# Kernel optimization log

Hardware: AMD Instinct MI355X
Metric: run time of the kernel (lower is better)

The kernel has to match this reference:

```python
import jax, jax.numpy as jnp
import numpy as np

NEG = -1000000.0

def setup_inputs() -> dict:
    key = jax.random.key(0)
    ks = jax.random.split(key, 7)
    B, Lq, Lk, Dq, Dk, Dv, H = 4, 256, 1024, 512, 512, 512, 256
    return {
        "query": jax.random.normal(ks[0], (B, Lq, Dq), dtype=jnp.float32),
        "key": jax.random.normal(ks[1], (B, Lk, Dk), dtype=jnp.float32),
        "value": jax.random.normal(ks[2], (B, Lk, Dv), dtype=jnp.float32),
        "valid_len": jax.random.randint(ks[3], (B,), 1, Lk + 1),
        "Wq": jax.random.normal(ks[4], (Dq, H), dtype=jnp.float32) * (1.0 / np.sqrt(Dq)),
        "Wk": jax.random.normal(ks[5], (Dk, H), dtype=jnp.float32) * (1.0 / np.sqrt(Dk)),
        "wv": jax.random.normal(ks[6], (H,), dtype=jnp.float32) * (1.0 / np.sqrt(H)),
    }

def reference(query, key, value, valid_len, Wq, Wk, wv):
    # projections: [B,Lq,H], [B,Lk,H]
    q = jnp.einsum("bqd,dh->bqh", query, Wq)
    k = jnp.einsum("bkd,dh->bkh", key, Wk)
    # broadcast-add + tanh: [B,Lq,Lk,H]
    features = jnp.tanh(q[:, :, None, :] + k[:, None, :, :])
    # score projection to scalar: [B,Lq,Lk]
    score = jnp.einsum("bqkh,h->bqk", features, wv)
    # masked softmax over keys (valid_len per batch, broadcast over queries)
    Lk = key.shape[1]
    mask = jnp.arange(Lk)[None, None, :] < valid_len[:, None, None]
    score = jnp.where(mask, score, NEG)
    attn = jax.nn.softmax(score, axis=-1)
    # weighted sum of values: [B,Lq,Dv]  (dropout is identity in eval)
    return jnp.einsum("bqk,bkv->bqv", attn, value)
```

## Files before the change

### kernel.cpp

```cpp
#include <hip/hip_runtime.h>

typedef __attribute__((ext_vector_type(8))) short short8v;
typedef __attribute__((ext_vector_type(4))) float float4v;
typedef unsigned int uint;

#define TWO_LOG2E 2.8853900817779268f
#define LOG2E     1.4426950408889634f

__device__ inline uint rne_bf16(float x) {
    uint u = __float_as_uint(x);
    return (u + 0x7fffu + ((u >> 16) & 1u)) >> 16;
}
__device__ inline uint pack_hi_lo(float a0, float a1, uint& lo_pack) {
    const uint h0 = rne_bf16(a0), h1 = rne_bf16(a1);
    const float f0 = __uint_as_float(h0 << 16), f1 = __uint_as_float(h1 << 16);
    const float l0 = a0 - f0, l1 = a1 - f1;
    lo_pack = (rne_bf16(l1) << 16) | rne_bf16(l0);
    return (h1 << 16) | h0;
}
__device__ inline void split8(const float4 x0, const float4 x1,
                              short8v& h, short8v& l) {
    const float xs[8] = {x0.x, x0.y, x0.z, x0.w, x1.x, x1.y, x1.z, x1.w};
    #pragma unroll
    for (int j = 0; j < 8; ++j) {
        const uint u = __float_as_uint(xs[j]);
        const uint hi = u & 0xFFFF0000u;
        const float lo = xs[j] - __uint_as_float(hi);
        h[j] = (short)(hi >> 16);
        l[j] = (short)rne_bf16(lo);
    }
}

__global__ __launch_bounds__(256) void prep_w(
    const float* __restrict__ Wq, const float* __restrict__ Wk,
    ushort* __restrict__ WT_hi, ushort* __restrict__ WT_lo)
{
    const int t = blockIdx.x * 256 + threadIdx.x;
    const int n = t & 255;
    const int kg = ((t >> 8) & 63) * 8;
    const int w = t >> 14;
    const float* W = w ? Wk : Wq;
    float x[8];
    #pragma unroll
    for (int i = 0; i < 8; ++i) x[i] = W[(size_t)(kg + i) * 256 + n];
    uint h0, h1, h2, h3, l0, l1, l2, l3;
    h0 = pack_hi_lo(x[0], x[1], l0);
    h1 = pack_hi_lo(x[2], x[3], l1);
    h2 = pack_hi_lo(x[4], x[5], l2);
    h3 = pack_hi_lo(x[6], x[7], l3);
    const size_t off = ((size_t)w * 256 + n) * 512 + kg;
    *(uint4*)(WT_hi + off) = make_uint4(h0, h1, h2, h3);
    *(uint4*)(WT_lo + off) = make_uint4(l0, l1, l2, l3);
}

__global__ __launch_bounds__(256) void prep_v(
    const float* __restrict__ value, const int* __restrict__ vlen,
    ushort* __restrict__ VT_hi, ushort* __restrict__ VT_lo)
{
    __shared__ float t[64][69];
    const int b = blockIdx.z;
    const int k0 = blockIdx.y * 64, n0 = blockIdx.x * 64;
    const int kendB = (vlen[b] + 31) & ~31;
    if (k0 >= kendB) return;

    const int tid = threadIdx.x;
    const int n_in = (tid & 15) * 4, k_in = tid >> 4;
    const float* src = value + ((size_t)b * 1024 + k0 + k_in) * 512 + n0 + n_in;
    #pragma unroll
    for (int p = 0; p < 4; ++p) {
        const float4 x = *(const float4*)(src + (size_t)p * 16 * 512);
        t[k_in + p * 16][n_in + 0] = x.x;
        t[k_in + p * 16][n_in + 1] = x.y;
        t[k_in + p * 16][n_in + 2] = x.z;
        t[k_in + p * 16][n_in + 3] = x.w;
    }
    __syncthreads();

    const int rn = tid >> 2, c0 = (tid & 3) * 16;
    uint hp[8], lp[8];
    #pragma unroll
    for (int i = 0; i < 8; ++i)
        hp[i] = pack_hi_lo(t[c0 + 2 * i][rn], t[c0 + 2 * i + 1][rn], lp[i]);
    const size_t off = ((size_t)b * 512 + n0 + rn) * 1024 + k0 + c0;
    *(uint4*)(VT_hi + off) = make_uint4(hp[0], hp[1], hp[2], hp[3]);
    *(uint4*)(VT_hi + off + 8) = make_uint4(hp[4], hp[5], hp[6], hp[7]);
    *(uint4*)(VT_lo + off) = make_uint4(lp[0], lp[1], lp[2], lp[3]);
    *(uint4*)(VT_lo + off + 8) = make_uint4(lp[4], lp[5], lp[6], lp[7]);
}

#define LOADA(s, kbase) { const int ko = (kbase) + half * 8;                   \
    _Pragma("unroll") for (int f = 0; f < 2; ++f) {                            \
        const float4 x0 = *(const float4*)(a_f + (size_t)(f * 16) * 512 + ko); \
        const float4 x1 = *(const float4*)(a_f + (size_t)(f * 16) * 512 + ko + 4); \
        split8(x0, x1, ah##s[f], al##s[f]); } }

#define LOADB(s, kbase) { const int ko = (kbase) + half * 8;                   \
    _Pragma("unroll") for (int f = 0; f < 4; ++f) {                            \
        bh##s[f] = *(const short8v*)(wt_h + (size_t)(f * 16) * 512 + ko);      \
        bl##s[f] = *(const short8v*)(wt_l + (size_t)(f * 16) * 512 + ko); } }

#define MFMAS(s)                                                                          \
    _Pragma("unroll") for (int mf = 0; mf < 2; ++mf)                                      \
    _Pragma("unroll") for (int nf = 0; nf < 4; ++nf) {                                    \
        acc[mf][nf] = __builtin_amdgcn_mfma_f32_16x16x32_bf16(ah##s[mf], bh##s[nf], acc[mf][nf], 0, 0, 0); \
        acc[mf][nf] = __builtin_amdgcn_mfma_f32_16x16x32_bf16(ah##s[mf], bl##s[nf], acc[mf][nf], 0, 0, 0); \
        acc[mf][nf] = __builtin_amdgcn_mfma_f32_16x16x32_bf16(al##s[mf], bh##s[nf], acc[mf][nf], 0, 0, 0); }

__global__ __launch_bounds__(64) void proj_mfma(
    const float* __restrict__ query, const float* __restrict__ key,
    const ushort* __restrict__ WT_hi, const ushort* __restrict__ WT_lo,
    const int* __restrict__ valid_len,
    float* __restrict__ EqT, float* __restrict__ EkT)
{
    const int lane = threadIdx.x;
    const int n0 = blockIdx.x * 64;
    const int m0 = blockIdx.y * 32;
    const bool isq = (m0 < 1024);
    int b = 0, kk0 = 0;
    if (!isq) {
        kk0 = (m0 - 1024) & 1023;
        b = (m0 - 1024) >> 10;
        if (kk0 >= valid_len[b]) return;
    }
    const int r = lane & 15, half = lane >> 4;
    const size_t wsel = isq ? 0 : (size_t)256 * 512;
    const ushort* wt_h = WT_hi + wsel + (size_t)(n0 + r) * 512;
    const ushort* wt_l = WT_lo + wsel + (size_t)(n0 + r) * 512;
    const float* a_f = isq ? (query + (size_t)(m0 + r) * 512)
                           : (key + (size_t)(m0 - 1024 + r) * 512);

    float4v acc[2][4] = {{{0.f}}};
    short8v ah0[2], al0[2], bh0[4], bl0[4];
    short8v ah1[2], al1[2], bh1[4], bl1[4];

    LOADA(0, 0); LOADB(0, 0);
    for (int kt = 0; kt < 512; kt += 64) {
        LOADA(1, kt + 32); LOADB(1, kt + 32);
        MFMAS(0);
        if (kt + 64 < 512) { LOADA(0, kt + 64); LOADB(0, kt + 64); }
        MFMAS(1);
    }

    #pragma unroll
    for (int mf = 0; mf < 2; ++mf) {
        #pragma unroll
        for (int nf = 0; nf < 4; ++nf) {
            float4v e;
            #pragma unroll
            for (int i = 0; i < 4; ++i)
                e[i] = __builtin_amdgcn_exp2f(acc[mf][nf][i] * TWO_LOG2E);
            if (isq) {
                *(float4v*)(EqT + (size_t)(n0 + nf * 16 + r) * 1024 +
                            m0 + mf * 16 + half * 4) = e;
            } else {
                *(float4v*)(EkT + (size_t)(b * 256 + n0 + nf * 16 + r) * 1024 +
                            kk0 + mf * 16 + half * 4) = e;
            }
        }
    }
}

__global__ __launch_bounds__(256) void score_partial(
    const float* __restrict__ EqT, const float* __restrict__ EkT,
    const float* __restrict__ wv, const int* __restrict__ valid_len,
    float* __restrict__ P)
{
    __shared__ float eqs[64][16];
    __shared__ float wvs[64];

    const int orig = blockIdx.x;
    const int wgid = (orig & 7) * 128 + (orig >> 3);
    const int qt = wgid & 15;
    const int kt = (wgid >> 4) & 3;
    const int hq = (wgid >> 6) & 3;
    const int b  = wgid >> 8;

    const int vlen = valid_len[b];
    if (kt * 256 >= vlen) return;

    const int tid = threadIdx.x;
    const int kg = tid & 63, qg = tid >> 6;
    const int k0 = kt * 256 + kg * 4;
    const int q0 = qt * 16;
    const int h0 = hq * 64;

    if (tid < 64) wvs[tid] = wv[h0 + tid];
    {
        const int i = tid * 4;
        const int h = i >> 4, q = i & 15;
        *(float4*)&eqs[h][q] =
            *(const float4*)(EqT + (size_t)(h0 + h) * 1024 + b * 256 + q0 + q);
    }
    __syncthreads();

    float acc[4][4] = {};
    if (k0 < vlen) {
        const float* ekp = EkT + (size_t)(b * 256 + h0) * 1024 + k0;
        #pragma unroll 2
        for (int h = 0; h < 64; ++h) {
            const float4 ek = *(const float4*)(ekp + (size_t)h * 1024);
            const float4 eq = *(const float4*)&eqs[h][qg * 4];
            const float w = wvs[h];
            const float ekv[4] = {ek.x, ek.y, ek.z, ek.w};
            const float eqv[4] = {eq.x, eq.y, eq.z, eq.w};
            #pragma unroll
            for (int qi = 0; qi < 4; ++qi) {
                const float e = eqv[qi];
                acc[qi][0] = fmaf(w, __builtin_amdgcn_rcpf(fmaf(e, ekv[0], 1.f)), acc[qi][0]);
                acc[qi][1] = fmaf(w, __builtin_amdgcn_rcpf(fmaf(e, ekv[1], 1.f)), acc[qi][1]);
                acc[qi][2] = fmaf(w, __builtin_amdgcn_rcpf(fmaf(e, ekv[2], 1.f)), acc[qi][2]);
                acc[qi][3] = fmaf(w, __builtin_amdgcn_rcpf(fmaf(e, ekv[3], 1.f)), acc[qi][3]);
            }
        }
    }

    float* Pq = P + (size_t)hq * (1024 * 1024);
    #pragma unroll
    for (int qi = 0; qi < 4; ++qi) {
        float4 o;
        o.x = acc[qi][0]; o.y = acc[qi][1]; o.z = acc[qi][2]; o.w = acc[qi][3];
        *(float4*)(Pq + (size_t)(b * 256 + q0 + qg * 4 + qi) * 1024 + k0) = o;
    }
}

__global__ __launch_bounds__(1024) void softmax_kernel(
    const float* __restrict__ P, const int* __restrict__ valid_len,
    ushort* __restrict__ attn_hi, ushort* __restrict__ attn_lo)
{
    __shared__ float red[16][4];

    const int tid = threadIdx.x;
    const int b = blockIdx.x >> 6;
    const int q0 = (blockIdx.x & 63) << 2;

    const int vlen = valid_len[b];
    const int k = tid;
    const bool v = (k < vlen);

    float s[4], m[4];
    #pragma unroll
    for (int q = 0; q < 4; ++q) {
        const size_t off = (size_t)(b * 256 + q0 + q) * 1024 + k;
        s[q] = -2.f * (P[off] + P[off + 1048576] +
                       P[off + 2097152] + P[off + 3145728]);
        m[q] = v ? s[q] : -1e30f;
    }
    #pragma unroll
    for (int o = 32; o; o >>= 1) {
        #pragma unroll
        for (int q = 0; q < 4; ++q) m[q] = fmaxf(m[q], __shfl_xor(m[q], o));
    }
    const int wid = tid >> 6;
    if ((tid & 63) == 0) {
        #pragma unroll
        for (int q = 0; q < 4; ++q) red[wid][q] = m[q];
    }
    __syncthreads();
    #pragma unroll
    for (int q = 0; q < 4; ++q) {
        float mm = red[0][q];
        #pragma unroll
        for (int w = 1; w < 16; ++w) mm = fmaxf(mm, red[w][q]);
        m[q] = mm;
    }
    __syncthreads();

    float p[4], l[4];
    #pragma unroll
    for (int q = 0; q < 4; ++q) {
        p[q] = v ? __builtin_amdgcn_exp2f((s[q] - m[q]) * LOG2E) : 0.f;
        l[q] = p[q];
    }
    #pragma unroll
    for (int o = 32; o; o >>= 1) {
        #pragma unroll
        for (int q = 0; q < 4; ++q) l[q] += __shfl_xor(l[q], o);
    }
    if ((tid & 63) == 0) {
        #pragma unroll
        for (int q = 0; q < 4; ++q) red[wid][q] = l[q];
    }
    __syncthreads();
    #pragma unroll
    for (int q = 0; q < 4; ++q) {
        float ss = red[0][q];
        #pragma unroll
        for (int w = 1; w < 16; ++w) ss += red[w][q];
        const float a = p[q] * __builtin_amdgcn_rcpf(ss);
        const uint hi = rne_bf16(a);
        const float lo = a - __uint_as_float(hi << 16);
        const size_t off = (size_t)(b * 256 + q0 + q) * 1024 + k;
        attn_hi[off] = (ushort)hi;
        attn_lo[off] = (ushort)rne_bf16(lo);
    }
}

#define PVLOAD(s, ko) {                                   \
    ah##s = *(const short8v*)(ah_p + (ko));               \
    al##s = *(const short8v*)(al_p + (ko));               \
    bh0##s = *(const short8v*)(bh_p + (ko));              \
    bl0##s = *(const short8v*)(bl_p + (ko));              \
    bh1##s = *(const short8v*)(bh_p + 16 * 1024 + (ko));  \
    bl1##s = *(const short8v*)(bl_p + 16 * 1024 + (ko)); }

#define PVMFMA(s) {                                                              \
    acc0 = __builtin_amdgcn_mfma_f32_16x16x32_bf16(ah##s, bh0##s, acc0, 0, 0, 0); \
    acc0 = __builtin_amdgcn_mfma_f32_16x16x32_bf16(ah##s, bl0##s, acc0, 0, 0, 0); \
    acc0 = __builtin_amdgcn_mfma_f32_16x16x32_bf16(al##s, bh0##s, acc0, 0, 0, 0); \
    acc1 = __builtin_amdgcn_mfma_f32_16x16x32_bf16(ah##s, bh1##s, acc1, 0, 0, 0); \
    acc1 = __builtin_amdgcn_mfma_f32_16x16x32_bf16(ah##s, bl1##s, acc1, 0, 0, 0); \
    acc1 = __builtin_amdgcn_mfma_f32_16x16x32_bf16(al##s, bh1##s, acc1, 0, 0, 0); }

__global__ __launch_bounds__(256) void pv_mfma(
    const ushort* __restrict__ attn_hi, const ushort* __restrict__ attn_lo,
    const ushort* __restrict__ VT_hi, const ushort* __restrict__ VT_lo,
    const int* __restrict__ valid_len,
    float* __restrict__ out)
{
    const int orig = blockIdx.x;
    const int wgid = (orig & 7) * 32 + (orig >> 3);
    const int qb = wgid & 3;
    const int rest = wgid >> 2;
    const int b = rest & 3;
    const int nt = rest >> 2;

    const int wid = threadIdx.x >> 6, lane = threadIdx.x & 63;
    const int n0 = nt * 32;
    const int q0 = qb * 64 + wid * 16;
    const int r = lane & 15, half = lane >> 4;
    const int kend = (valid_len[b] + 31) & ~31;

    const ushort* ah_p = attn_hi + (size_t)(b * 256 + q0 + r) * 1024 + half * 8;
    const ushort* al_p = attn_lo + (size_t)(b * 256 + q0 + r) * 1024 + half * 8;
    const ushort* bh_p = VT_hi + (size_t)(b * 512 + n0 + r) * 1024 + half * 8;
    const ushort* bl_p = VT_lo + (size_t)(b * 512 + n0 + r) * 1024 + half * 8;

    float4v acc0 = {0.f}, acc1 = {0.f};
    short8v ah0, al0, bh00, bl00, bh10, bl10;
    short8v ah1, al1, bh01, bl01, bh11, bl11;

    PVLOAD(0, 0);
    for (int kt = 0; kt < kend; kt += 64) {
        if (kt + 32 < kend) PVLOAD(1, kt + 32);
        PVMFMA(0);
        if (kt + 64 < kend) PVLOAD(0, kt + 64);
        if (kt + 32 < kend) PVMFMA(1);
    }

    float* op = out + (size_t)b * 256 * 512 + (size_t)(q0 + half * 4) * 512 + n0 + r;
    #pragma unroll
    for (int i = 0; i < 4; ++i) {
        op[(size_t)i * 512] = acc0[i];
        op[(size_t)i * 512 + 16] = acc1[i];
    }
}

extern "C" void kernel_launch(void* const* d_in, const int* in_sizes, int n_in,
                              void* d_out, int out_size, void* d_ws, size_t ws_size,
                              hipStream_t stream)
{
    const float* query = (const float*)d_in[0];
    const float* key   = (const float*)d_in[1];
    const float* value = (const float*)d_in[2];
    const int*   vlen  = (const int*)d_in[3];
    const float* Wq    = (const float*)d_in[4];
    const float* Wk    = (const float*)d_in[5];
    const float* wv    = (const float*)d_in[6];
    float* out = (float*)d_out;

    float*  EqT     = (float*)d_ws;
    float*  EkT     = EqT + 262144;
    float*  P       = EkT + 1048576;
    ushort* WT_hi   = (ushort*)(P + 4194304);
    ushort* WT_lo   = WT_hi + 262144;
    ushort* attn_hi = WT_lo + 262144;
    ushort* attn_lo = attn_hi + 1048576;
    ushort* VT_hi   = attn_lo + 1048576;
    ushort* VT_lo   = VT_hi + 2097152;

    hipLaunchKernelGGL(prep_w, dim3(128), dim3(256), 0, stream,
                       Wq, Wk, WT_hi, WT_lo);
    hipLaunchKernelGGL(prep_v, dim3(8, 16, 4), dim3(256), 0, stream,
                       value, vlen, VT_hi, VT_lo);
    hipLaunchKernelGGL(proj_mfma, dim3(4, 160), dim3(64), 0, stream,
                       query, key, WT_hi, WT_lo, vlen, EqT, EkT);
    hipLaunchKernelGGL(score_partial, dim3(1024), dim3(256), 0, stream,
                       EqT, EkT, wv, vlen, P);
    hipLaunchKernelGGL(softmax_kernel, dim3(256), dim3(1024), 0, stream,
                       P, vlen, attn_hi, attn_lo);
    hipLaunchKernelGGL(pv_mfma, dim3(256), dim3(256), 0, stream,
                       attn_hi, attn_lo, VT_hi, VT_lo, vlen, out);
}
```

Measured before the change: 93.02 us.

## Tile EkT by key block, prefetch Ek rows in registers, remap score grid

The projection kernel now writes the exponentiated key projections in a tiled layout [b][ktile][h][256], so each score block reads a contiguous 256-float stride per head instead of a 1024-float stride. The score kernel prefetches eight Ek rows ahead into a register ring buffer and fully unrolls the head loop to hide global load latency. The block-to-work mapping is also changed so consecutive blocks share query/head data with kt fastest. This raises register pressure from the unrolled loop and buffer, and the new block order may change L2 locality and XCD distribution.

```diff
diff --git a/kernel.cpp b/kernel.cpp
--- a/kernel.cpp
+++ b/kernel.cpp
@@ -110,7 +110,7 @@
     const float* __restrict__ query, const float* __restrict__ key,
     const ushort* __restrict__ WT_hi, const ushort* __restrict__ WT_lo,
     const int* __restrict__ valid_len,
-    float* __restrict__ EqT, float* __restrict__ EkT)
+    float* __restrict__ EqT, float* __restrict__ EkT2)
 {
     const int lane = threadIdx.x;
     const int n0 = blockIdx.x * 64;
@@ -153,27 +153,29 @@
                 *(float4v*)(EqT + (size_t)(n0 + nf * 16 + r) * 1024 +
                             m0 + mf * 16 + half * 4) = e;
             } else {
-                *(float4v*)(EkT + (size_t)(b * 256 + n0 + nf * 16 + r) * 1024 +
-                            kk0 + mf * 16 + half * 4) = e;
+                const int kidx = kk0 + mf * 16 + half * 4;
+                const int ktile = kidx >> 8, kloc = kidx & 255;
+                const int h = n0 + nf * 16 + r;
+                *(float4v*)(EkT2 +
+                    ((size_t)(b * 4 + ktile) * 256 + h) * 256 + kloc) = e;
             }
         }
     }
 }
 
 __global__ __launch_bounds__(256) void score_partial(
-    const float* __restrict__ EqT, const float* __restrict__ EkT,
+    const float* __restrict__ EqT, const float* __restrict__ EkT2,
     const float* __restrict__ wv, const int* __restrict__ valid_len,
     float* __restrict__ P)
 {
     __shared__ float eqs[64][16];
     __shared__ float wvs[64];
 
-    const int orig = blockIdx.x;
-    const int wgid = (orig & 7) * 128 + (orig >> 3);
-    const int qt = wgid & 15;
-    const int kt = (wgid >> 4) & 3;
-    const int hq = (wgid >> 6) & 3;
-    const int b  = wgid >> 8;
+    const int wgid = blockIdx.x;
+    const int kt = wgid & 3;
+    const int b  = (wgid >> 2) & 3;
+    const int hq = (wgid >> 4) & 3;
+    const int qt = wgid >> 6;
 
     const int vlen = valid_len[b];
     if (kt * 256 >= vlen) return;
@@ -195,10 +197,19 @@
 
     float acc[4][4] = {};
     if (k0 < vlen) {
-        const float* ekp = EkT + (size_t)(b * 256 + h0) * 1024 + k0;
-        #pragma unroll 2
+        const float* ekp = EkT2 +
+            ((size_t)(b * 4 + kt) * 256 + h0) * 256 + kg * 4;
+
+        float4 ekbuf[8];
+        #pragma unroll
+        for (int i = 0; i < 8; ++i)
+            ekbuf[i] = *(const float4*)(ekp + (size_t)i * 256);
+
+        #pragma unroll
         for (int h = 0; h < 64; ++h) {
-            const float4 ek = *(const float4*)(ekp + (size_t)h * 1024);
+            const float4 ek = ekbuf[h & 7];
+            if (h + 8 < 64)
+                ekbuf[h & 7] = *(const float4*)(ekp + (size_t)(h + 8) * 256);
             const float4 eq = *(const float4*)&eqs[h][qg * 4];
             const float w = wvs[h];
             const float ekv[4] = {ek.x, ek.y, ek.z, ek.w};
@@ -369,8 +380,8 @@
     float* out = (float*)d_out;
 
     float*  EqT     = (float*)d_ws;
-    float*  EkT     = EqT + 262144;
-    float*  P       = EkT + 1048576;
+    float*  EkT2    = EqT + 262144;
+    float*  P       = EkT2 + 1048576;
     ushort* WT_hi   = (ushort*)(P + 4194304);
     ushort* WT_lo   = WT_hi + 262144;
     ushort* attn_hi = WT_lo + 262144;
@@ -383,9 +394,9 @@
     hipLaunchKernelGGL(prep_v, dim3(8, 16, 4), dim3(256), 0, stream,
                        value, vlen, VT_hi, VT_lo);
     hipLaunchKernelGGL(proj_mfma, dim3(4, 160), dim3(64), 0, stream,
-                       query, key, WT_hi, WT_lo, vlen, EqT, EkT);
+                       query, key, WT_hi, WT_lo, vlen, EqT, EkT2);
     hipLaunchKernelGGL(score_partial, dim3(1024), dim3(256), 0, stream,
-                       EqT, EkT, wv, vlen, P);
+                       EqT, EkT2, wv, vlen, P);
     hipLaunchKernelGGL(softmax_kernel, dim3(256), dim3(1024), 0, stream,
                        P, vlen, attn_hi, attn_lo);
     hipLaunchKernelGGL(pv_mfma, dim3(256), dim3(256), 0, stream,
```

Measured after the change: 113.3 us. 21.8% more time.
